# Kernel tuning notes

Hardware: AMD Instinct MI355X
Metric: run time of the kernel (lower is better)

## Reference

```python
import jax, jax.numpy as jnp
import numpy as np

DIM = 512
HEADS = 8
DIM_HEAD = 64
INNER = HEADS * DIM_HEAD  # 512
SCALE = DIM_HEAD ** -0.5


def setup_inputs() -> dict:
    key = jax.random.key(0)
    k1, k2, k3, k4 = jax.random.split(key, 4)
    x = jax.random.normal(k1, (4, 2048, DIM), dtype=jnp.float32)
    # Dense(inner_dim*3, use_bias=False): weight [dim, 3*inner]
    w_qkv = jax.random.normal(k2, (DIM, 3 * INNER), dtype=jnp.float32) * (DIM ** -0.5)
    # to_out Dense(dim): weight [inner, dim] + bias [dim]
    w_out = jax.random.normal(k3, (INNER, DIM), dtype=jnp.float32) * (INNER ** -0.5)
    b_out = jax.random.normal(k4, (DIM,), dtype=jnp.float32) * 0.01
    return {"x": x, "w_qkv": w_qkv, "w_out": w_out, "b_out": b_out}


def reference(x, w_qkv, w_out, b_out):
    b, n, _ = x.shape
    qkv = x @ w_qkv                                  # [b, n, 3*inner]
    q, k, v = jnp.split(qkv, 3, axis=-1)             # each [b, n, inner]
    def to_heads(t):
        return t.reshape(b, n, HEADS, DIM_HEAD).transpose(0, 2, 1, 3)  # [b, h, n, d]
    q, k, v = map(to_heads, (q, k, v))
    dots = jnp.einsum('bhid,bhjd->bhij', q, k) * SCALE
    attn = jax.nn.softmax(dots, axis=-1)
    out = jnp.einsum('bhij,bhjd->bhid', attn, v)     # [b, h, n, d]
    out = out.transpose(0, 2, 1, 3).reshape(b, n, INNER)
    return out @ w_out + b_out                       # [b, n, dim]
```

## Files before the change

kernel.cpp:

```cpp
#include <hip/hip_runtime.h>
#include <stdint.h>

#define DIM    512
#define HEADS  8
#define DHEAD  64
#define SEQ    2048
#define BATCH  4
#define BH     (BATCH*HEADS)
#define MROWS  (BATCH*SEQ)
#define NQKV   (3*DIM)
#define QSCALE 0.18033688011112042f

typedef __bf16 bf16x8 __attribute__((ext_vector_type(8)));
typedef float  f32x4  __attribute__((ext_vector_type(4)));
typedef float  f32x16 __attribute__((ext_vector_type(16)));

typedef unsigned short u16;

#if __has_builtin(__builtin_amdgcn_exp2f)
#define EXP2(x) __builtin_amdgcn_exp2f(x)
#else
#define EXP2(x) exp2f(x)
#endif

__device__ __forceinline__ u16 f2bf(float f) {
    union { float f; uint32_t u; } v; v.f = f;
    uint32_t u = v.u;
    uint32_t r = (u + 0x7FFFu + ((u >> 16) & 1u)) >> 16;
    return (u16)r;
}
__device__ __forceinline__ float bf2f(u16 h) {
    union { uint32_t u; float f; } v; v.u = ((uint32_t)h) << 16;
    return v.f;
}
__device__ __forceinline__ uint32_t pk2bf(float a, float b) {
    union { float f; uint32_t u; } ua, ub; ua.f = a; ub.f = b;
#if __has_builtin(__builtin_amdgcn_perm)
    return __builtin_amdgcn_perm(ub.u + 0x8000u, ua.u + 0x8000u, 0x07060302u);
#else
    return ((ua.u + 0x8000u) >> 16) | ((ub.u + 0x8000u) & 0xFFFF0000u);
#endif
}
__device__ __forceinline__ uint32_t cvtpk(float a, float b) {
    uint32_t r;
    asm("v_cvt_pk_bf16_f32 %0, %1, %2" : "=v"(r) : "v"(a), "v"(b));
    return r;
}

#define P32SWAP(x, y) asm("v_permlane32_swap_b32 %0, %1" : "+v"(x), "+v"(y))

__device__ __forceinline__ void async16(const void* g, u16* l) {
    __builtin_amdgcn_global_load_lds(
        (const __attribute__((address_space(1))) void*)g,
        (__attribute__((address_space(3))) void*)l, 16, 0, 0);
}

#define XBLKS (MROWS * DIM / 4 / 256)
#define WQT   ((DIM / 64) * (NQKV / 64))
#define WOT   ((DIM / 64) * (DIM / 64))
__global__ void prep(const void* __restrict__ x, const void* __restrict__ wq,
                     const void* __restrict__ wo, u16* __restrict__ xb,
                     u16* __restrict__ wtq, u16* __restrict__ wto,
                     int* __restrict__ flag) {
    __shared__ int cnt;
    __shared__ __align__(16) u16 tile[64][72];
    int tid = threadIdx.x;
    if (tid == 0) cnt = 0;
    __syncthreads();
    {
        u16 v = ((const u16*)x)[tid * 2];
        int e = (v >> 7) & 0xFF;
        atomicAdd(&cnt, (v == 0) || (e >= 100 && e <= 140));
    }
    __syncthreads();
    int isbf = (cnt >= 192);
    int b = blockIdx.x;
    if (b == 0 && tid == 0) *flag = isbf;

    if (b < XBLKS) {
        int i = b * 256 + tid;
        if (isbf) {
            ((uint2*)xb)[i] = ((const uint2*)x)[i];
        } else {
            float4 v = ((const float4*)x)[i];
            ushort4 o;
            o.x = f2bf(v.x); o.y = f2bf(v.y); o.z = f2bf(v.z); o.w = f2bf(v.w);
            ((ushort4*)xb)[i] = o;
        }
        return;
    }
    const void* W; u16* Wt; int N, tb;
    if (b < XBLKS + WQT) { W = wq; Wt = wtq; N = NQKV; tb = b - XBLKS; }
    else                 { W = wo; Wt = wto; N = DIM;  tb = b - XBLKS - WQT; }
    int tn = N / 64;
    int k0 = (tb / tn) * 64, n0 = (tb - (tb / tn) * tn) * 64;

#pragma unroll 4
    for (int it = 0; it < 16; ++it) {
        int idx = it * 256 + tid;
        int r = idx >> 6, c = idx & 63;
        u16 v = isbf ? ((const u16*)W)[(size_t)(k0 + r) * N + n0 + c]
                     : f2bf(((const float*)W)[(size_t)(k0 + r) * N + n0 + c]);
        tile[c][r] = v;
    }
    __syncthreads();
    {
        int n = tid >> 2, ks = (tid & 3) * 16;
        uint4 v0 = *(const uint4*)&tile[n][ks];
        uint4 v1 = *(const uint4*)&tile[n][ks + 8];
        *(uint4*)&Wt[(size_t)(n0 + n) * DIM + k0 + ks] = v0;
        *(uint4*)&Wt[(size_t)(n0 + n) * DIM + k0 + ks + 8] = v1;
    }
}

template<int KDIM, int TM, int TN>
__device__ __forceinline__ void gemm_lds_db(
        const u16* __restrict__ A, const u16* __restrict__ Bt,
        int m0, int n0, int tid, u16* As, u16* Bs,
        f32x4 (&acc)[TM / 32][TN / 32]) {
    int lane = tid & 63, ln = lane & 15, quad = lane >> 4, w = tid >> 6;
    int wm = (w >> 1) * (TM / 2), wn = (w & 1) * (TN / 2);

    auto stage = [&](int buf, int k0) {
#pragma unroll
        for (int ii = 0; ii < TM / 64; ++ii) {
            int r0 = (ii * 4 + w) * 16;
            int row = r0 + (lane >> 2);
            int seg = (lane & 3) ^ (row & 3);
            async16(A + (size_t)(m0 + row) * KDIM + k0 + seg * 8,
                    As + buf * TM * 32 + r0 * 32);
        }
#pragma unroll
        for (int ii = 0; ii < TN / 64; ++ii) {
            int r0 = (ii * 4 + w) * 16;
            int row = r0 + (lane >> 2);
            int seg = (lane & 3) ^ (row & 3);
            async16(Bt + (size_t)(n0 + row) * KDIM + k0 + seg * 8,
                    Bs + buf * TN * 32 + r0 * 32);
        }
    };

    stage(0, 0);
#pragma unroll 1
    for (int kk = 0; kk < KDIM / 32; ++kk) {
        __syncthreads();
        if (kk + 1 < KDIM / 32) stage((kk + 1) & 1, (kk + 1) * 32);
        const u16* Ac = As + (kk & 1) * TM * 32;
        const u16* Bc = Bs + (kk & 1) * TN * 32;
        bf16x8 a[TM / 32], b[TN / 32];
        int rseg = (quad ^ (ln & 3)) * 8;
#pragma unroll
        for (int i = 0; i < TM / 32; ++i)
            a[i] = *(const bf16x8*)(Ac + (wm + i * 16 + ln) * 32 + rseg);
#pragma unroll
        for (int j = 0; j < TN / 32; ++j)
            b[j] = *(const bf16x8*)(Bc + (wn + j * 16 + ln) * 32 + rseg);
#pragma unroll
        for (int i = 0; i < TM / 32; ++i)
#pragma unroll
            for (int j = 0; j < TN / 32; ++j)
                acc[i][j] = __builtin_amdgcn_mfma_f32_16x16x32_bf16(
                    a[i], b[j], acc[i][j], 0, 0, 0);
    }
}

__global__ __launch_bounds__(256, 3) void qkv_gemm(
        const u16* __restrict__ X, const u16* __restrict__ Wt,
        u16* __restrict__ Qt, u16* __restrict__ Kb, u16* __restrict__ Vt) {
    __shared__ __align__(16) u16 SM[16384];
    u16* As = SM;
    u16* Bs = SM + 8192;

    int tid  = threadIdx.x;
    int lane = tid & 63, ln = lane & 15, quad = lane >> 4, wid = tid >> 6;
    int m0 = blockIdx.x * 128, n0 = blockIdx.y * 128;
    int wm = (wid >> 1) * 64, wn = (wid & 1) * 64;

    f32x4 acc[4][4];
#pragma unroll
    for (int i = 0; i < 4; ++i)
#pragma unroll
        for (int j = 0; j < 4; ++j) acc[i][j] = 0.f;

    gemm_lds_db<DIM, 128, 128>(X, Wt, m0, n0, tid, As, Bs, acc);

    int which = n0 >> 9;
    if (which == 1) {
#pragma unroll
        for (int j = 0; j < 4; ++j) {
            int col = n0 + wn + j * 16 + ln;
            int hd  = col & 511;
            int h   = hd >> 6, d = hd & 63;
#pragma unroll
            for (int i = 0; i < 4; ++i) {
                int rbase = m0 + wm + i * 16 + quad * 4;
                int b = rbase >> 11, n = rbase & 2047;
                int bh = b * HEADS + h;
#pragma unroll
                for (int r = 0; r < 4; ++r)
                    Kb[((size_t)bh * SEQ + n + r) * DHEAD + d] = f2bf(acc[i][j][r]);
            }
        }
        return;
    }

    float sc = (which == 0) ? QSCALE : 1.0f;
    u16* dst = (which == 0) ? Qt : Vt;
    int nhd0 = n0 & 511;
    __syncthreads();

#pragma unroll
    for (int j = 0; j < 4; ++j) {
        int cl = wn + j * 16 + ln;
        int sw = (cl & 7) << 5;
#pragma unroll
        for (int i = 0; i < 4; ++i) {
            int row = wm + i * 16 + quad * 4;
            uint2 pv;
            pv.x = pk2bf(acc[i][j][0] * sc, acc[i][j][1] * sc);
            pv.y = pk2bf(acc[i][j][2] * sc, acc[i][j][3] * sc);
            *(uint2*)((char*)SM + (cl << 8) + ((row << 1) ^ sw)) = pv;
        }
    }
    __syncthreads();

    int b = m0 >> 11;
    int nbase = m0 & 2047;
#pragma unroll
    for (int it = 0; it < 8; ++it) {
        int col  = wid * 32 + it * 4 + quad;
        int gcol = nhd0 + col;
        int h = gcol >> 6, d = gcol & 63;
        uint4 v = *(const uint4*)((const char*)SM +
                                  (col << 8) + ((ln << 4) ^ ((col & 7) << 5)));
        *(uint4*)&dst[((size_t)(b * HEADS + h) * DHEAD + d) * SEQ + nbase + ln * 8] = v;
    }
}

__global__ __launch_bounds__(512, 4) void flash_attn(
        const u16* __restrict__ Qt, const u16* __restrict__ Kb,
        const u16* __restrict__ Vt, u16* __restrict__ Ob) {
    __shared__ __align__(16) u16 SMEM[24576];
    __shared__ float Lcomb[4][32];
    u16* Kc0 = SMEM;
    u16* Vc0 = SMEM + 12288;
    float* OC = (float*)SMEM;

    int tid  = threadIdx.x;
    int lane = tid & 63, c = lane & 31, hi = lane >> 5, wid = tid >> 6;
    int ws = wid & 1, wq = wid >> 1;
    int bh = blockIdx.x;
    int q0 = blockIdx.y * 128 + wq * 32;

    const u16* Qh = Qt + (size_t)bh * SEQ * DHEAD;
    const u16* Kh = Kb + (size_t)bh * SEQ * DHEAD;
    const u16* Vh = Vt + (size_t)bh * DHEAD * SEQ;

    int srow = lane >> 3;
    auto stageKV = [&](int buf, int kc) {
        int slab = wid;
        int g = (lane & 7) ^ srow ^ (slab & 3);
        const u16* gk = Kh + (size_t)(kc + slab * 8 + srow) * DHEAD + g * 8;
        async16(gk, Kc0 + buf * 4096 + slab * 8 * 64);
        const u16* gv = Vh + (size_t)(slab * 8 + srow) * SEQ + kc + g * 8;
        async16(gv, Vc0 + buf * 4096 + slab * 8 * 64);
    };

    bf16x8 qf[4];
#pragma unroll
    for (int ds = 0; ds < 4; ++ds) {
        union { u16 a[8]; bf16x8 v; } u;
#pragma unroll
        for (int j = 0; j < 8; ++j)
            u.a[j] = Qh[(size_t)(ds * 16 + hi * 8 + j) * SEQ + q0 + c];
        qf[ds] = u.v;
    }

    bf16x8 onesf;
    { union { uint32_t d[4]; bf16x8 v; } u;
      u.d[0] = u.d[1] = u.d[2] = u.d[3] = 0x3F803F80u; onesf = u.v; }

    f32x16 o[2];
    f32x16 lacc;
    lacc = 0.f;
#pragma unroll
    for (int dt = 0; dt < 2; ++dt) o[dt] = 0.f;

    stageKV(0, 0);
    stageKV(1, 64);

    int fl = (c & 7) ^ ((c >> 3) & 3);
    int cur = 0;

#pragma unroll 1
    for (int kc = 0; kc < SEQ; kc += 64) {
        if (kc + 64 < SEQ) asm volatile("s_waitcnt vmcnt(2)" ::: "memory");
        else               asm volatile("s_waitcnt vmcnt(0)" ::: "memory");
        __builtin_amdgcn_s_barrier();
        __builtin_amdgcn_sched_barrier(0);
        if (kc + 128 < SEQ) stageKV((cur + 2) % 3, kc + 128);

        const u16* Kcur = Kc0 + cur * 4096;
        const u16* Vcur = Vc0 + cur * 4096;

        bf16x8 kf[4];
#pragma unroll
        for (int ds = 0; ds < 4; ++ds) {
            int slot = (ds * 2 + hi) ^ fl;
            kf[ds] = *(const bf16x8*)&Kcur[(ws * 32 + c) * 64 + slot * 8];
        }

        f32x16 s;
        s = 0.f;
        __builtin_amdgcn_s_setprio(1);
#pragma unroll
        for (int ds = 0; ds < 4; ++ds)
            s = __builtin_amdgcn_mfma_f32_32x32x16_bf16(
                kf[ds], qf[ds], s, 0, 0, 0);
        __builtin_amdgcn_s_setprio(0);

        float p[16];
#pragma unroll
        for (int r = 0; r < 16; ++r) p[r] = EXP2(s[r]);
        uint32_t X[8];
#pragma unroll
        for (int i = 0; i < 8; ++i) X[i] = cvtpk(p[2 * i], p[2 * i + 1]);
        P32SWAP(X[0], X[2]); P32SWAP(X[1], X[3]);
        P32SWAP(X[4], X[6]); P32SWAP(X[5], X[7]);
        bf16x8 pa[2];
        union { uint32_t d[4]; bf16x8 v; } u0, u1;
        u0.d[0] = X[0]; u0.d[1] = X[1]; u0.d[2] = X[2]; u0.d[3] = X[3];
        u1.d[0] = X[4]; u1.d[1] = X[5]; u1.d[2] = X[6]; u1.d[3] = X[7];
        pa[0] = u0.v; pa[1] = u1.v;

        __builtin_amdgcn_s_setprio(1);
#pragma unroll
        for (int tl = 0; tl < 2; ++tl) {
#pragma unroll
            for (int dt = 0; dt < 2; ++dt) {
                int slot = ((ws * 2 + tl) * 2 + hi) ^ fl;
                bf16x8 vf = *(const bf16x8*)&Vcur[(dt * 32 + c) * 64 + slot * 8];
                o[dt] = __builtin_amdgcn_mfma_f32_32x32x16_bf16(
                    pa[tl], vf, o[dt], 0, 0, 0);
            }
            lacc = __builtin_amdgcn_mfma_f32_32x32x16_bf16(
                pa[tl], onesf, lacc, 0, 0, 0);
        }
        __builtin_amdgcn_s_setprio(0);

        cur = (cur == 2) ? 0 : cur + 1;
    }

    __syncthreads();

    if (ws == 1) {
#pragma unroll
        for (int dt = 0; dt < 2; ++dt) {
            int base = (((wq * 2 + dt) * 2 + hi) * 32 + c) * 18;
#pragma unroll
            for (int g = 0; g < 4; ++g) {
                f32x4 v;
                v[0] = o[dt][g * 4 + 0]; v[1] = o[dt][g * 4 + 1];
                v[2] = o[dt][g * 4 + 2]; v[3] = o[dt][g * 4 + 3];
                *(f32x4*)&OC[base + g * 4] = v;
            }
        }
        if (c == 0) {
#pragma unroll
            for (int r = 0; r < 16; ++r)
                Lcomb[wq][(r & 3) + 8 * (r >> 2) + 4 * hi] = lacc[r];
        }
    }
    __syncthreads();

    if (ws == 0) {
        int b = bh >> 3, hh = bh & 7;
#pragma unroll
        for (int dt = 0; dt < 2; ++dt) {
            int base = (((wq * 2 + dt) * 2 + hi) * 32 + c) * 18;
#pragma unroll
            for (int g = 0; g < 4; ++g) {
                f32x4 v = *(const f32x4*)&OC[base + g * 4];
                o[dt][g * 4 + 0] += v[0]; o[dt][g * 4 + 1] += v[1];
                o[dt][g * 4 + 2] += v[2]; o[dt][g * 4 + 3] += v[3];
            }
        }
        f32x16 linv;
#pragma unroll
        for (int r = 0; r < 16; ++r)
            linv[r] = 1.0f / (lacc[r] + Lcomb[wq][(r & 3) + 8 * (r >> 2) + 4 * hi]);
#pragma unroll
        for (int dt = 0; dt < 2; ++dt)
#pragma unroll
            for (int r = 0; r < 16; ++r) {
                int ql = (r & 3) + 8 * (r >> 2) + 4 * hi;
                int n  = q0 + ql;
                int d  = dt * 32 + c;
                Ob[((size_t)(b * SEQ + n)) * DIM + hh * DHEAD + d] =
                    f2bf(o[dt][r] * linv[r]);
            }
    }
}

__global__ __launch_bounds__(256, 3) void out_gemm(
        const u16* __restrict__ A, const u16* __restrict__ Wt,
        const void* __restrict__ bias, void* __restrict__ out,
        const int* __restrict__ flag) {
    __shared__ __align__(16) u16 As[2 * 64 * 32];
    __shared__ __align__(16) u16 Bs[2 * 128 * 32];

    int tid  = threadIdx.x;
    int lane = tid & 63, ln = lane & 15, quad = lane >> 4, wid = tid >> 6;
    int m0 = blockIdx.x * 64, n0 = blockIdx.y * 128;
    int wm = (wid >> 1) * 32, wn = (wid & 1) * 64;
    int isbf = *flag;

    f32x4 acc[2][4];
#pragma unroll
    for (int i = 0; i < 2; ++i)
#pragma unroll
        for (int j = 0; j < 4; ++j) acc[i][j] = 0.f;

    gemm_lds_db<DIM, 64, 128>(A, Wt, m0, n0, tid, As, Bs, acc);

#pragma unroll
    for (int j = 0; j < 4; ++j) {
        int col = n0 + wn + j * 16 + ln;
        float bv = isbf ? bf2f(((const u16*)bias)[col])
                        : ((const float*)bias)[col];
#pragma unroll
        for (int i = 0; i < 2; ++i) {
            int rbase = m0 + wm + i * 16 + quad * 4;
#pragma unroll
            for (int r = 0; r < 4; ++r) {
                int row = rbase + r;
                size_t off = (size_t)row * DIM + col;
                float val = acc[i][j][r] + bv;
                if (isbf) ((u16*)out)[off] = f2bf(val);
                else      ((float*)out)[off] = val;
            }
        }
    }
}

extern "C" void kernel_launch(void* const* d_in, const int* in_sizes, int n_in,
                              void* d_out, int out_size, void* d_ws, size_t ws_size,
                              hipStream_t stream) {
    const void* x     = d_in[0];
    const void* w_qkv = d_in[1];
    const void* w_out = d_in[2];
    const void* b_out = d_in[3];

    int* flag   = (int*)d_ws;
    u16* x_bf   = (u16*)((char*)d_ws + 16);
    u16* wt_qkv = x_bf + (size_t)MROWS * DIM;
    u16* wt_out = wt_qkv + (size_t)NQKV * DIM;
    u16* Qt     = wt_out + (size_t)DIM * DIM;
    u16* Kb     = Qt + (size_t)BH * SEQ * DHEAD;
    u16* Vt     = Kb + (size_t)BH * SEQ * DHEAD;
    u16* attn   = x_bf;

    prep<<<XBLKS + WQT + WOT, 256, 0, stream>>>(
        x, w_qkv, w_out, x_bf, wt_qkv, wt_out, flag);
    qkv_gemm<<<dim3(MROWS / 128, NQKV / 128), 256, 0, stream>>>(x_bf, wt_qkv, Qt, Kb, Vt);
    flash_attn<<<dim3(BH, SEQ / 128), 512, 0, stream>>>(Qt, Kb, Vt, attn);
    out_gemm<<<dim3(MROWS / 64, DIM / 128), 256, 0, stream>>>(attn, wt_out, b_out, d_out, flag);
}
```

Measured before the change: 179.0 us.

## Fuse fp32-to-bf16 conversion of x into QKV GEMM loader

```diff
diff --git a/kernel.cpp b/kernel.cpp
--- a/kernel.cpp
+++ b/kernel.cpp
@@ -41,6 +41,9 @@
     return ((ua.u + 0x8000u) >> 16) | ((ub.u + 0x8000u) & 0xFFFF0000u);
 #endif
 }
+__device__ __forceinline__ uint32_t pk2bf_rne(float a, float b) {
+    return (uint32_t)f2bf(a) | ((uint32_t)f2bf(b) << 16);
+}
 __device__ __forceinline__ uint32_t cvtpk(float a, float b) {
     uint32_t r;
     asm("v_cvt_pk_bf16_f32 %0, %1, %2" : "=v"(r) : "v"(a), "v"(b));
@@ -55,11 +58,10 @@
         (__attribute__((address_space(3))) void*)l, 16, 0, 0);
 }
 
-#define XBLKS (MROWS * DIM / 4 / 256)
 #define WQT   ((DIM / 64) * (NQKV / 64))
 #define WOT   ((DIM / 64) * (DIM / 64))
 __global__ void prep(const void* __restrict__ x, const void* __restrict__ wq,
-                     const void* __restrict__ wo, u16* __restrict__ xb,
+                     const void* __restrict__ wo,
                      u16* __restrict__ wtq, u16* __restrict__ wto,
                      int* __restrict__ flag) {
     __shared__ int cnt;
@@ -77,21 +79,9 @@
     int b = blockIdx.x;
     if (b == 0 && tid == 0) *flag = isbf;
 
-    if (b < XBLKS) {
-        int i = b * 256 + tid;
-        if (isbf) {
-            ((uint2*)xb)[i] = ((const uint2*)x)[i];
-        } else {
-            float4 v = ((const float4*)x)[i];
-            ushort4 o;
-            o.x = f2bf(v.x); o.y = f2bf(v.y); o.z = f2bf(v.z); o.w = f2bf(v.w);
-            ((ushort4*)xb)[i] = o;
-        }
-        return;
-    }
     const void* W; u16* Wt; int N, tb;
-    if (b < XBLKS + WQT) { W = wq; Wt = wtq; N = NQKV; tb = b - XBLKS; }
-    else                 { W = wo; Wt = wto; N = DIM;  tb = b - XBLKS - WQT; }
+    if (b < WQT) { W = wq; Wt = wtq; N = NQKV; tb = b; }
+    else         { W = wo; Wt = wto; N = DIM;  tb = b - WQT; }
     int tn = N / 64;
     int k0 = (tb / tn) * 64, n0 = (tb - (tb / tn) * tn) * 64;
 
@@ -165,8 +155,9 @@
 }
 
 __global__ __launch_bounds__(256, 3) void qkv_gemm(
-        const u16* __restrict__ X, const u16* __restrict__ Wt,
-        u16* __restrict__ Qt, u16* __restrict__ Kb, u16* __restrict__ Vt) {
+        const void* __restrict__ x, const u16* __restrict__ Wt,
+        u16* __restrict__ Qt, u16* __restrict__ Kb, u16* __restrict__ Vt,
+        const int* __restrict__ flag) {
     __shared__ __align__(16) u16 SM[16384];
     u16* As = SM;
     u16* Bs = SM + 8192;
@@ -175,6 +166,40 @@
     int lane = tid & 63, ln = lane & 15, quad = lane >> 4, wid = tid >> 6;
     int m0 = blockIdx.x * 128, n0 = blockIdx.y * 128;
     int wm = (wid >> 1) * 64, wn = (wid & 1) * 64;
+    int isbf = *flag;
+
+    auto stageA = [&](int buf, int k0) {
+#pragma unroll
+        for (int ii = 0; ii < 2; ++ii) {
+            int r0 = (ii * 4 + wid) * 16;
+            int row = r0 + (lane >> 2);
+            int g = (lane & 3) ^ (row & 3);
+            if (isbf) {
+                async16((const u16*)x + (size_t)(m0 + row) * DIM + k0 + g * 8,
+                        As + buf * 4096 + r0 * 32);
+            } else {
+                const float* src = (const float*)x + (size_t)(m0 + row) * DIM + k0 + g * 8;
+                float4 v0 = *(const float4*)src;
+                float4 v1 = *(const float4*)(src + 4);
+                uint4 d;
+                d.x = pk2bf_rne(v0.x, v0.y);
+                d.y = pk2bf_rne(v0.z, v0.w);
+                d.z = pk2bf_rne(v1.x, v1.y);
+                d.w = pk2bf_rne(v1.z, v1.w);
+                *(uint4*)(As + buf * 4096 + r0 * 32 + (lane >> 2) * 32 + (lane & 3) * 8) = d;
+            }
+        }
+    };
+    auto stageB = [&](int buf, int k0) {
+#pragma unroll
+        for (int ii = 0; ii < 2; ++ii) {
+            int r0 = (ii * 4 + wid) * 16;
+            int row = r0 + (lane >> 2);
+            int g = (lane & 3) ^ (row & 3);
+            async16(Wt + (size_t)(n0 + row) * DIM + k0 + g * 8,
+                    Bs + buf * 4096 + r0 * 32);
+        }
+    };
 
     f32x4 acc[4][4];
 #pragma unroll
@@ -182,7 +207,29 @@
 #pragma unroll
         for (int j = 0; j < 4; ++j) acc[i][j] = 0.f;
 
-    gemm_lds_db<DIM, 128, 128>(X, Wt, m0, n0, tid, As, Bs, acc);
+    stageA(0, 0); stageB(0, 0);
+#pragma unroll 1
+    for (int kk = 0; kk < 16; ++kk) {
+        __syncthreads();
+        if (kk + 1 < 16) { stageA((kk + 1) & 1, (kk + 1) * 32);
+                           stageB((kk + 1) & 1, (kk + 1) * 32); }
+        const u16* Ac = As + (kk & 1) * 4096;
+        const u16* Bc = Bs + (kk & 1) * 4096;
+        bf16x8 a[4], b[4];
+        int rseg = (quad ^ (ln & 3)) * 8;
+#pragma unroll
+        for (int i = 0; i < 4; ++i)
+            a[i] = *(const bf16x8*)(Ac + (wm + i * 16 + ln) * 32 + rseg);
+#pragma unroll
+        for (int j = 0; j < 4; ++j)
+            b[j] = *(const bf16x8*)(Bc + (wn + j * 16 + ln) * 32 + rseg);
+#pragma unroll
+        for (int i = 0; i < 4; ++i)
+#pragma unroll
+            for (int j = 0; j < 4; ++j)
+                acc[i][j] = __builtin_amdgcn_mfma_f32_16x16x32_bf16(
+                    a[i], b[j], acc[i][j], 0, 0, 0);
+    }
 
     int which = n0 >> 9;
     if (which == 1) {
@@ -194,8 +241,8 @@
 #pragma unroll
             for (int i = 0; i < 4; ++i) {
                 int rbase = m0 + wm + i * 16 + quad * 4;
-                int b = rbase >> 11, n = rbase & 2047;
-                int bh = b * HEADS + h;
+                int b2 = rbase >> 11, n = rbase & 2047;
+                int bh = b2 * HEADS + h;
 #pragma unroll
                 for (int r = 0; r < 4; ++r)
                     Kb[((size_t)bh * SEQ + n + r) * DHEAD + d] = f2bf(acc[i][j][r]);
@@ -224,7 +271,7 @@
     }
     __syncthreads();
 
-    int b = m0 >> 11;
+    int b2 = m0 >> 11;
     int nbase = m0 & 2047;
 #pragma unroll
     for (int it = 0; it < 8; ++it) {
@@ -233,7 +280,7 @@
         int h = gcol >> 6, d = gcol & 63;
         uint4 v = *(const uint4*)((const char*)SM +
                                   (col << 8) + ((ln << 4) ^ ((col & 7) << 5)));
-        *(uint4*)&dst[((size_t)(b * HEADS + h) * DHEAD + d) * SEQ + nbase + ln * 8] = v;
+        *(uint4*)&dst[((size_t)(b2 * HEADS + h) * DHEAD + d) * SEQ + nbase + ln * 8] = v;
     }
 }
 
@@ -452,17 +499,18 @@
     const void* b_out = d_in[3];
 
     int* flag   = (int*)d_ws;
-    u16* x_bf   = (u16*)((char*)d_ws + 16);
-    u16* wt_qkv = x_bf + (size_t)MROWS * DIM;
+    u16* attn   = (u16*)((char*)d_ws + 16);
+    u16* wt_qkv = attn + (size_t)MROWS * DIM;
     u16* wt_out = wt_qkv + (size_t)NQKV * DIM;
     u16* Qt     = wt_out + (size_t)DIM * DIM;
     u16* Kb     = Qt + (size_t)BH * SEQ * DHEAD;
     u16* Vt     = Kb + (size_t)BH * SEQ * DHEAD;
-    u16* attn   = x_bf;
-
-    prep<<<XBLKS + WQT + WOT, 256, 0, stream>>>(
-        x, w_qkv, w_out, x_bf, wt_qkv, wt_out, flag);
-    qkv_gemm<<<dim3(MROWS / 128, NQKV / 128), 256, 0, stream>>>(x_bf, wt_qkv, Qt, Kb, Vt);
+
+    prep<<<WQT + WOT, 256, 0, stream>>>(
+        x, w_qkv, w_out, wt_qkv, wt_out, flag);
+    qkv_gemm<<<dim3(MROWS / 128, NQKV / 128), 256, 0, stream>>>(
+        x, wt_qkv, Qt, Kb, Vt, flag);
     flash_attn<<<dim3(BH, SEQ / 128), 512, 0, stream>>>(Qt, Kb, Vt, attn);
-    out_gemm<<<dim3(MROWS / 64, DIM / 128), 256, 0, stream>>>(attn, wt_out, b_out, d_out, flag);
-}
+    out_gemm<<<dim3(MROWS / 64, DIM / 128), 256, 0, stream>>>(
+        attn, wt_out, b_out, d_out, flag);
+}
```

Measured after the change: 171.4 us, median of 2. -4.3%, faster.
